# Optimization experiments

Hardware: AMD Instinct MI355X
Metric: run time of the kernel (lower is better)

The kernel has to match this reference:

```python
import jax, jax.numpy as jnp
import numpy as np

N = 30000          # nodes
R = 8              # relations
NUM_BASES = 30     # basis decomposition (fixed in module)
IN_DIM = 256
Z_DIM = 128
HID = Z_DIM * 2
E = N * 16         # edges (avg degree 16)


def setup_inputs() -> dict:
    key = jax.random.key(0)
    ks = jax.random.split(key, 12)
    x = jax.random.normal(ks[0], (N, IN_DIM), jnp.float32)
    edge_index = jax.random.randint(ks[1], (2, E), 0, N, dtype=jnp.int64)
    edge_type = jax.random.randint(ks[2], (E,), 0, R, dtype=jnp.int64)
    s1 = 1.0 / np.sqrt(IN_DIM)
    s2 = 1.0 / np.sqrt(HID)
    sb = 1.0 / np.sqrt(NUM_BASES)
    bases1 = jax.random.normal(ks[3], (NUM_BASES, IN_DIM, HID), jnp.float32) * s1
    comp1 = jax.random.normal(ks[4], (R, NUM_BASES), jnp.float32) * sb
    root1 = jax.random.normal(ks[5], (IN_DIM, HID), jnp.float32) * s1
    bias1 = jnp.zeros((HID,), jnp.float32)
    bases2 = jax.random.normal(ks[6], (NUM_BASES, HID, Z_DIM), jnp.float32) * s2
    comp2 = jax.random.normal(ks[7], (R, NUM_BASES), jnp.float32) * sb
    root2 = jax.random.normal(ks[8], (HID, Z_DIM), jnp.float32) * s2
    bias2 = jnp.zeros((Z_DIM,), jnp.float32)
    return dict(x=x, edge_index=edge_index, edge_type=edge_type,
                bases1=bases1, comp1=comp1, root1=root1, bias1=bias1,
                bases2=bases2, comp2=comp2, root2=root2, bias2=bias2)


def _rgcn_layer(x, src, dst, etype, bases, comp, root, bias):
    # weight[r] = sum_b comp[r,b] * bases[b]  (basis decomposition)
    n = x.shape[0]
    W = jnp.einsum('rb,bio->rio', comp, bases)          # [R, in, out]
    xall = jnp.einsum('ni,rio->nro', x, W)              # [N, R, out] dense transform
    msg = xall[src, etype]                              # [E, out] gather per edge
    seg = dst * R + etype                               # segment = (dst, relation)
    sums = jax.ops.segment_sum(msg, seg, num_segments=n * R)
    cnt = jax.ops.segment_sum(jnp.ones((msg.shape[0],), msg.dtype), seg,
                              num_segments=n * R)
    mean = sums / jnp.maximum(cnt, 1.0)[:, None]        # PyG RGCNConv aggr='mean'
    agg = mean.reshape(n, R, -1).sum(axis=1)            # sum over relations
    return agg + x @ root + bias


def reference(x, edge_index, edge_type, bases1, comp1, root1, bias1,
              bases2, comp2, root2, bias2):
    src, dst = edge_index[0], edge_index[1]
    z = _rgcn_layer(x, src, dst, edge_type, bases1, comp1, root1, bias1)
    z = jax.nn.leaky_relu(z, negative_slope=0.01)
    z = _rgcn_layer(z, src, dst, edge_type, bases2, comp2, root2, bias2)
    return z
```

## Files before the change

kernel.cpp:

```cpp
#include <hip/hip_runtime.h>
#include <hip/hip_bf16.h>
#include <stdint.h>

#define NN     30000
#define MPAD   30080
#define RR     8
#define NBASES 30
#define KD     256
#define EE     480000
#define NSEG   (NN * RR)
#define BK     64
#define CAP    32
#define NC1    2304
#define NC2    1152

typedef unsigned short u16;
typedef __attribute__((ext_vector_type(8))) short bf16x8;
typedef __attribute__((ext_vector_type(4))) float f32x4;

__device__ __forceinline__ u16 f2b(float f) {
  union { float f; uint32_t u; } v; v.f = f;
  return (u16)((v.u + 0x7fffu + ((v.u >> 16) & 1u)) >> 16);
}
__device__ __forceinline__ float b2f(u16 h) {
  union { uint32_t u; float f; } v; v.u = ((uint32_t)h) << 16;
  return v.f;
}

__device__ __forceinline__ void gl_lds16(const void* g, void* l) {
  __builtin_amdgcn_global_load_lds((__attribute__((address_space(1))) void*)g,
                                   (__attribute__((address_space(3))) void*)l,
                                   16, 0, 0);
}

template<int N>
__device__ __forceinline__ void waitcnt_vm() {
  asm volatile("s_waitcnt vmcnt(%0)" :: "n"(N) : "memory");
}

template<int NCOLS>
__global__ __launch_bounds__(512, 2)
void k_gemm_y(const u16* __restrict__ A, const u16* __restrict__ Bn,
              u16* __restrict__ Y) {
  constexpr int NT = 128, MT = 128;
  constexpr int MI = 2, NI = 4;
  constexpr int NKI = KD / BK;
  __shared__ __align__(16) char smem[65536];
  u16 (*Alds)[MT * BK] = (u16(*)[MT * BK])smem;
  u16 (*Blds)[NT * BK] = (u16(*)[NT * BK])(smem + 2 * MT * BK * 2);
  float* eps = (float*)smem;
  const int tid = threadIdx.x;
  const int w = tid >> 6, lane = tid & 63;
  const int bn = blockIdx.x * NT, bm = blockIdx.y * MT;
  const int wm = (w >> 1) * 32;
  const int wn = (w & 1) * 64;
  const int l15 = lane & 15, l4 = lane >> 4;

  f32x4 acc[MI][NI];
  #pragma unroll
  for (int mi = 0; mi < MI; ++mi)
    #pragma unroll
    for (int ni = 0; ni < NI; ++ni) acc[mi][ni] = (f32x4){0.f, 0.f, 0.f, 0.f};

  auto stage = [&](int buf, int k0) {
    #pragma unroll
    for (int it = 0; it < 2; ++it) {
      int chb = it * 512 + w * 64;
      int ch = chb + lane;
      int row = ch >> 3, pc = ch & 7;
      int lc = pc ^ (row & 7);
      gl_lds16(&A[(size_t)(bm + row) * KD + k0 + lc * 8], &Alds[buf][chb * 8]);
    }
    #pragma unroll
    for (int it = 0; it < 2; ++it) {
      int chb = it * 512 + w * 64;
      int ch = chb + lane;
      int row = ch >> 3, pc = ch & 7;
      int lc = pc ^ (row & 7);
      gl_lds16(&Bn[(size_t)(bn + row) * KD + k0 + lc * 8], &Blds[buf][chb * 8]);
    }
  };

  stage(0, 0);
  int buf = 0;
  for (int t = 0; t < NKI; ++t) {
    if (t + 1 < NKI) {
      stage(buf ^ 1, (t + 1) * BK);
      waitcnt_vm<4>();
    } else {
      waitcnt_vm<0>();
    }
    __builtin_amdgcn_s_barrier();
    __builtin_amdgcn_sched_barrier(0);
    #pragma unroll
    for (int s = 0; s < 2; ++s) {
      bf16x8 av[MI], bv[NI];
      #pragma unroll
      for (int mi = 0; mi < MI; ++mi) {
        int row = wm + mi * 16 + l15;
        int pc = (4 * s + l4) ^ (row & 7);
        av[mi] = *(const bf16x8*)&Alds[buf][row * BK + pc * 8];
      }
      #pragma unroll
      for (int ni = 0; ni < NI; ++ni) {
        int row = wn + ni * 16 + l15;
        int pc = (4 * s + l4) ^ (row & 7);
        bv[ni] = *(const bf16x8*)&Blds[buf][row * BK + pc * 8];
      }
      #pragma unroll
      for (int mi = 0; mi < MI; ++mi)
        #pragma unroll
        for (int ni = 0; ni < NI; ++ni)
          acc[mi][ni] = __builtin_amdgcn_mfma_f32_16x16x32_bf16(av[mi], bv[ni], acc[mi][ni], 0, 0, 0);
    }
    asm volatile("s_waitcnt lgkmcnt(0)" ::: "memory");
    __builtin_amdgcn_s_barrier();
    buf ^= 1;
  }

  #pragma unroll
  for (int p = 0; p < 2; ++p) {
    if ((wm >> 6) == p) {
      #pragma unroll
      for (int mi = 0; mi < MI; ++mi)
        #pragma unroll
        for (int ni = 0; ni < NI; ++ni) {
          int col = wn + ni * 16 + l15;
          #pragma unroll
          for (int v = 0; v < 4; ++v) {
            int row = (wm & 63) + mi * 16 + l4 * 4 + v;
            eps[row * 132 + col] = acc[mi][ni][v];
          }
        }
    }
    __syncthreads();
    {
      int row = tid >> 3, oc = tid & 7;
      const float* src = &eps[row * 132 + oc * 16];
      uint4 o[2];
      #pragma unroll
      for (int hh = 0; hh < 2; ++hh) {
        float f0 = src[hh*8+0], f1 = src[hh*8+1], f2 = src[hh*8+2], f3 = src[hh*8+3];
        float f4 = src[hh*8+4], f5 = src[hh*8+5], f6 = src[hh*8+6], f7 = src[hh*8+7];
        o[hh].x = ((uint32_t)f2b(f1) << 16) | (uint32_t)f2b(f0);
        o[hh].y = ((uint32_t)f2b(f3) << 16) | (uint32_t)f2b(f2);
        o[hh].z = ((uint32_t)f2b(f5) << 16) | (uint32_t)f2b(f4);
        o[hh].w = ((uint32_t)f2b(f7) << 16) | (uint32_t)f2b(f6);
      }
      u16* dst = &Y[(size_t)(bm + p * 64 + row) * NCOLS + bn + oc * 16];
      *(uint4*)dst = o[0];
      *(uint4*)(dst + 8) = o[1];
    }
    __syncthreads();
  }
}

template<int D, bool LAST>
__global__ __launch_bounds__(256)
void k_agg(const u16* __restrict__ Y, const int* __restrict__ cnt,
           const int* __restrict__ esrc, const float* __restrict__ bias,
           u16* __restrict__ ob, float* __restrict__ of) {
  constexpr int YW = 9 * D;
  constexpr int CW = D / 32;
  const int tid = threadIdx.x;
  const int h = tid >> 5, ln = tid & 31;
  const int d = blockIdx.x * 8 + h;

  int cn[8];
  {
    int4 c0 = *(const int4*)&cnt[d << 3];
    int4 c1 = *(const int4*)&cnt[(d << 3) + 4];
    cn[0]=c0.x; cn[1]=c0.y; cn[2]=c0.z; cn[3]=c0.w;
    cn[4]=c1.x; cn[5]=c1.y; cn[6]=c1.z; cn[7]=c1.w;
  }
  int4 q[8];
  #pragma unroll
  for (int r = 0; r < 8; ++r)
    q[r] = *(const int4*)&esrc[((d << 3) + r) * CAP];

  float a[CW];
  #pragma unroll
  for (int j = 0; j < CW; ++j) a[j] = 0.f;

  #pragma unroll
  for (int r = 0; r < 8; ++r) {
    int n = cn[r] < CAP ? cn[r] : CAP;
    if (n == 0) continue;
    float t[CW];
    #pragma unroll
    for (int j = 0; j < CW; ++j) t[j] = 0.f;
    const int qsrc[4] = {q[r].x, q[r].y, q[r].z, q[r].w};
    #pragma unroll
    for (int e = 0; e < 4; ++e) {
      if (e < n) {
        int sr = qsrc[e];
        if constexpr (CW == 8) {
          uint4 v = *(const uint4*)&Y[(size_t)sr * YW + r * D + ln * 8];
          t[0]+=b2f((u16)v.x); t[1]+=b2f((u16)(v.x>>16));
          t[2]+=b2f((u16)v.y); t[3]+=b2f((u16)(v.y>>16));
          t[4]+=b2f((u16)v.z); t[5]+=b2f((u16)(v.z>>16));
          t[6]+=b2f((u16)v.w); t[7]+=b2f((u16)(v.w>>16));
        } else {
          uint2 v = *(const uint2*)&Y[(size_t)sr * YW + r * D + ln * 4];
          t[0]+=b2f((u16)v.x); t[1]+=b2f((u16)(v.x>>16));
          t[2]+=b2f((u16)v.y); t[3]+=b2f((u16)(v.y>>16));
        }
      }
    }
    #pragma unroll 1
    for (int e = 4; e < n; ++e) {
      int sr = esrc[((d << 3) + r) * CAP + e];
      if constexpr (CW == 8) {
        uint4 v = *(const uint4*)&Y[(size_t)sr * YW + r * D + ln * 8];
        t[0]+=b2f((u16)v.x); t[1]+=b2f((u16)(v.x>>16));
        t[2]+=b2f((u16)v.y); t[3]+=b2f((u16)(v.y>>16));
        t[4]+=b2f((u16)v.z); t[5]+=b2f((u16)(v.z>>16));
        t[6]+=b2f((u16)v.w); t[7]+=b2f((u16)(v.w>>16));
      } else {
        uint2 v = *(const uint2*)&Y[(size_t)sr * YW + r * D + ln * 4];
        t[0]+=b2f((u16)v.x); t[1]+=b2f((u16)(v.x>>16));
        t[2]+=b2f((u16)v.y); t[3]+=b2f((u16)(v.y>>16));
      }
    }
    float inv = 1.f / (float)n;
    #pragma unroll
    for (int j = 0; j < CW; ++j) a[j] = fmaf(inv, t[j], a[j]);
  }

  if constexpr (CW == 8) {
    uint4 sv = *(const uint4*)&Y[(size_t)d * YW + 8 * D + ln * 8];
    float s[8] = { b2f((u16)sv.x), b2f((u16)(sv.x>>16)),
                   b2f((u16)sv.y), b2f((u16)(sv.y>>16)),
                   b2f((u16)sv.z), b2f((u16)(sv.z>>16)),
                   b2f((u16)sv.w), b2f((u16)(sv.w>>16)) };
    float4 b0 = *(const float4*)&bias[ln * 8];
    float4 b1 = *(const float4*)&bias[ln * 8 + 4];
    float vv[8];
    vv[0]=a[0]+s[0]+b0.x; vv[1]=a[1]+s[1]+b0.y;
    vv[2]=a[2]+s[2]+b0.z; vv[3]=a[3]+s[3]+b0.w;
    vv[4]=a[4]+s[4]+b1.x; vv[5]=a[5]+s[5]+b1.y;
    vv[6]=a[6]+s[6]+b1.z; vv[7]=a[7]+s[7]+b1.w;
    if (!LAST) {
      #pragma unroll
      for (int j = 0; j < 8; ++j) vv[j] = vv[j] > 0.f ? vv[j] : 0.01f * vv[j];
      uint4 o;
      o.x = ((uint32_t)f2b(vv[1]) << 16) | (uint32_t)f2b(vv[0]);
      o.y = ((uint32_t)f2b(vv[3]) << 16) | (uint32_t)f2b(vv[2]);
      o.z = ((uint32_t)f2b(vv[5]) << 16) | (uint32_t)f2b(vv[4]);
      o.w = ((uint32_t)f2b(vv[7]) << 16) | (uint32_t)f2b(vv[6]);
      *(uint4*)&ob[(size_t)d * KD + ln * 8] = o;
    } else {
      float4 o0 = {vv[0], vv[1], vv[2], vv[3]};
      float4 o1 = {vv[4], vv[5], vv[6], vv[7]};
      *(float4*)&of[(size_t)d * 256 + ln * 8] = o0;
      *(float4*)&of[(size_t)d * 256 + ln * 8 + 4] = o1;
    }
  } else {
    uint2 sv = *(const uint2*)&Y[(size_t)d * YW + 8 * D + ln * 4];
    float s[4] = { b2f((u16)sv.x), b2f((u16)(sv.x>>16)),
                   b2f((u16)sv.y), b2f((u16)(sv.y>>16)) };
    float4 b0 = *(const float4*)&bias[ln * 4];
    float vv[4];
    vv[0]=a[0]+s[0]+b0.x; vv[1]=a[1]+s[1]+b0.y;
    vv[2]=a[2]+s[2]+b0.z; vv[3]=a[3]+s[3]+b0.w;
    if (!LAST) {
      #pragma unroll
      for (int j = 0; j < 4; ++j) vv[j] = vv[j] > 0.f ? vv[j] : 0.01f * vv[j];
      uint2 o;
      o.x = ((uint32_t)f2b(vv[1]) << 16) | (uint32_t)f2b(vv[0]);
      o.y = ((uint32_t)f2b(vv[3]) << 16) | (uint32_t)f2b(vv[2]);
      *(uint2*)&ob[(size_t)d * KD + ln * 4] = o;
    } else {
      float4 o = {vv[0], vv[1], vv[2], vv[3]};
      *(float4*)&of[(size_t)d * 128 + ln * 4] = o;
    }
  }
}

__global__ void k_cast_x(const float* __restrict__ x, u16* __restrict__ xb) {
  int t = blockIdx.x * 256 + threadIdx.x;
  if (t < NN * KD / 4) {
    float4 v = ((const float4*)x)[t];
    union { u16 h[4]; uint2 u; } p;
    p.h[0] = f2b(v.x); p.h[1] = f2b(v.y); p.h[2] = f2b(v.z); p.h[3] = f2b(v.w);
    ((uint2*)xb)[t] = p.u;
  }
}

__global__ void k_combineT1(const float* __restrict__ bases, const float* __restrict__ comp,
                            const float* __restrict__ root, u16* __restrict__ Bn) {
  int i = blockIdx.x, rg = blockIdx.y, o = threadIdx.x;
  float v; int j;
  if (rg < RR) {
    float acc = 0.f;
    #pragma unroll
    for (int b = 0; b < NBASES; ++b)
      acc += comp[rg * NBASES + b] * bases[(size_t)b * 65536 + i * 256 + o];
    v = acc; j = rg * 256 + o;
  } else {
    v = root[i * 256 + o]; j = 2048 + o;
  }
  Bn[(size_t)j * KD + i] = f2b(v);
}

__global__ void k_combineT2(const float* __restrict__ bases, const float* __restrict__ comp,
                            const float* __restrict__ root, u16* __restrict__ Bn) {
  int i = blockIdx.x, rg = blockIdx.y, o = threadIdx.x;
  float v; int j;
  if (rg < RR) {
    float acc = 0.f;
    #pragma unroll
    for (int b = 0; b < NBASES; ++b)
      acc += comp[rg * NBASES + b] * bases[(size_t)b * 32768 + i * 128 + o];
    v = acc; j = rg * 128 + o;
  } else {
    v = root[i * 128 + o]; j = 1024 + o;
  }
  Bn[(size_t)j * KD + i] = f2b(v);
}

__global__ void k_bucket_fs(const int* __restrict__ ei, const int* __restrict__ ety,
                            int* __restrict__ cnt, int* __restrict__ esrc) {
  int e = blockIdx.x * 256 + threadIdx.x;
  if (e < EE) {
    int seg = ei[EE + e] * RR + ety[e];
    int pos = atomicAdd(&cnt[seg], 1);
    if (pos < CAP) esrc[seg * CAP + pos] = ei[e];
  }
}

extern "C" void kernel_launch(void* const* d_in, const int* in_sizes, int n_in,
                              void* d_out, int out_size, void* d_ws, size_t ws_size,
                              hipStream_t stream) {
  const float* x      = (const float*)d_in[0];
  const int*   ei     = (const int*)d_in[1];
  const int*   ety    = (const int*)d_in[2];
  const float* bases1 = (const float*)d_in[3];
  const float* comp1  = (const float*)d_in[4];
  const float* root1  = (const float*)d_in[5];
  const float* bias1  = (const float*)d_in[6];
  const float* bases2 = (const float*)d_in[7];
  const float* comp2  = (const float*)d_in[8];
  const float* root2  = (const float*)d_in[9];
  const float* bias2  = (const float*)d_in[10];
  float* out = (float*)d_out;

  char* p = (char*)d_ws;
  auto alloc = [&](size_t bytes) {
    char* q = p; p += (bytes + 255) & ~(size_t)255; return q;
  };
  u16* Y    = (u16*)alloc((size_t)MPAD * NC1 * 2);
  u16* xb   = (u16*)alloc((size_t)MPAD * KD * 2);
  u16* z1b  = (u16*)alloc((size_t)MPAD * KD * 2);
  u16* Bn1  = (u16*)alloc((size_t)NC1 * KD * 2);
  u16* Bn2  = (u16*)alloc((size_t)NC2 * KD * 2);
  int* cnt  = (int*)alloc((size_t)NSEG * 4);
  int* esrc = (int*)alloc((size_t)NSEG * CAP * 4);

  hipMemsetAsync(cnt, 0, (size_t)NSEG * 4, stream);
  k_bucket_fs<<<(EE + 255) / 256, 256, 0, stream>>>(ei, ety, cnt, esrc);

  k_cast_x<<<NN * KD / 4 / 256, 256, 0, stream>>>(x, xb);
  k_combineT1<<<dim3(256, 9), 256, 0, stream>>>(bases1, comp1, root1, Bn1);
  k_combineT2<<<dim3(256, 9), 128, 0, stream>>>(bases2, comp2, root2, Bn2);

  k_gemm_y<NC1><<<dim3(NC1 / 128, MPAD / 128), 512, 0, stream>>>(xb, Bn1, Y);
  k_agg<256, false><<<NN / 8, 256, 0, stream>>>(Y, cnt, esrc, bias1, z1b, nullptr);

  k_gemm_y<NC2><<<dim3(NC2 / 128, MPAD / 128), 512, 0, stream>>>(z1b, Bn2, Y);
  k_agg<128, true><<<NN / 8, 256, 0, stream>>>(Y, cnt, esrc, bias2, nullptr, out);
}
```

Measured before the change: 327.7 us.

## Triple-buffer GEMM K-loop with smaller K tile and new LDS swizzle

The GEMM kernel's K tile shrinks from 64 to 32 and its LDS ring grows from two to three buffers, so loads are issued two iterations ahead. This cuts shared memory per block from 64KB to 48KB and raises the launch-bounds occupancy hint from 2 to 6. The aim is to hide global-load latency and fit more blocks per CU. The cost is twice as many barrier-synchronised iterations, and the 6-block hint may force register spilling with 512-thread blocks.

```diff
diff --git a/kernel.cpp b/kernel.cpp
--- a/kernel.cpp
+++ b/kernel.cpp
@@ -9,7 +9,6 @@
 #define KD     256
 #define EE     480000
 #define NSEG   (NN * RR)
-#define BK     64
 #define CAP    32
 #define NC1    2304
 #define NC2    1152
@@ -39,15 +38,16 @@
 }
 
 template<int NCOLS>
-__global__ __launch_bounds__(512, 2)
+__global__ __launch_bounds__(512, 6)
 void k_gemm_y(const u16* __restrict__ A, const u16* __restrict__ Bn,
               u16* __restrict__ Y) {
   constexpr int NT = 128, MT = 128;
   constexpr int MI = 2, NI = 4;
-  constexpr int NKI = KD / BK;
-  __shared__ __align__(16) char smem[65536];
-  u16 (*Alds)[MT * BK] = (u16(*)[MT * BK])smem;
-  u16 (*Blds)[NT * BK] = (u16(*)[NT * BK])(smem + 2 * MT * BK * 2);
+  constexpr int BKL = 32;
+  constexpr int NKI = KD / BKL;
+  __shared__ __align__(16) char smem[49152];
+  u16 (*Alds)[MT * BKL] = (u16(*)[MT * BKL])smem;
+  u16 (*Blds)[NT * BKL] = (u16(*)[NT * BKL])(smem + 3 * MT * BKL * 2);
   float* eps = (float*)smem;
   const int tid = threadIdx.x;
   const int w = tid >> 6, lane = tid & 63;
@@ -55,6 +55,9 @@
   const int wm = (w >> 1) * 32;
   const int wn = (w & 1) * 64;
   const int l15 = lane & 15, l4 = lane >> 4;
+  const int grow = tid >> 2;
+  const int gpc = tid & 3;
+  const int glc = (gpc - (grow >> 1)) & 3;
 
   f32x4 acc[MI][NI];
   #pragma unroll
@@ -63,49 +66,37 @@
     for (int ni = 0; ni < NI; ++ni) acc[mi][ni] = (f32x4){0.f, 0.f, 0.f, 0.f};
 
   auto stage = [&](int buf, int k0) {
-    #pragma unroll
-    for (int it = 0; it < 2; ++it) {
-      int chb = it * 512 + w * 64;
-      int ch = chb + lane;
-      int row = ch >> 3, pc = ch & 7;
-      int lc = pc ^ (row & 7);
-      gl_lds16(&A[(size_t)(bm + row) * KD + k0 + lc * 8], &Alds[buf][chb * 8]);
-    }
-    #pragma unroll
-    for (int it = 0; it < 2; ++it) {
-      int chb = it * 512 + w * 64;
-      int ch = chb + lane;
-      int row = ch >> 3, pc = ch & 7;
-      int lc = pc ^ (row & 7);
-      gl_lds16(&Bn[(size_t)(bn + row) * KD + k0 + lc * 8], &Blds[buf][chb * 8]);
-    }
+    gl_lds16(&A[(size_t)(bm + grow) * KD + k0 + glc * 8], &Alds[buf][w * 512]);
+    gl_lds16(&Bn[(size_t)(bn + grow) * KD + k0 + glc * 8], &Blds[buf][w * 512]);
   };
 
   stage(0, 0);
-  int buf = 0;
+  stage(1, BKL);
   for (int t = 0; t < NKI; ++t) {
-    if (t + 1 < NKI) {
-      stage(buf ^ 1, (t + 1) * BK);
+    const int bc = t % 3;
+    if (t + 2 < NKI) {
+      stage((t + 2) % 3, (t + 2) * BKL);
       waitcnt_vm<4>();
+    } else if (t + 1 < NKI) {
+      waitcnt_vm<2>();
     } else {
       waitcnt_vm<0>();
     }
     __builtin_amdgcn_s_barrier();
     __builtin_amdgcn_sched_barrier(0);
-    #pragma unroll
-    for (int s = 0; s < 2; ++s) {
+    {
       bf16x8 av[MI], bv[NI];
       #pragma unroll
       for (int mi = 0; mi < MI; ++mi) {
         int row = wm + mi * 16 + l15;
-        int pc = (4 * s + l4) ^ (row & 7);
-        av[mi] = *(const bf16x8*)&Alds[buf][row * BK + pc * 8];
+        int pc = (l4 + (row >> 1)) & 3;
+        av[mi] = *(const bf16x8*)&Alds[bc][row * BKL + pc * 8];
       }
       #pragma unroll
       for (int ni = 0; ni < NI; ++ni) {
         int row = wn + ni * 16 + l15;
-        int pc = (4 * s + l4) ^ (row & 7);
-        bv[ni] = *(const bf16x8*)&Blds[buf][row * BK + pc * 8];
+        int pc = (l4 + (row >> 1)) & 3;
+        bv[ni] = *(const bf16x8*)&Blds[bc][row * BKL + pc * 8];
       }
       #pragma unroll
       for (int mi = 0; mi < MI; ++mi)
@@ -115,7 +106,6 @@
     }
     asm volatile("s_waitcnt lgkmcnt(0)" ::: "memory");
     __builtin_amdgcn_s_barrier();
-    buf ^= 1;
   }
 
   #pragma unroll
```

Result: no change. 328.5 us (+0.3%).

## Merge prep kernels into one launch and use nontemporal stores for GEMM output

Applied to the files above, without the earlier changes.

The four preprocessing kernels (x cast, two basis-combine transposes and edge bucketing) are folded into a single kernel that dispatches on block index ranges. This removes three launch gaps and lets the independent pieces run at the same time. Separately, the GEMM epilogue now writes Y with nontemporal stores, meant to reduce cache pollution from the large intermediate. The risk is that Y is read back soon by the aggregation kernel, so bypassing cache could hurt reuse.

```diff
diff --git a/kernel.cpp b/kernel.cpp
--- a/kernel.cpp
+++ b/kernel.cpp
@@ -17,6 +17,7 @@
 typedef unsigned short u16;
 typedef __attribute__((ext_vector_type(8))) short bf16x8;
 typedef __attribute__((ext_vector_type(4))) float f32x4;
+typedef __attribute__((ext_vector_type(4))) unsigned int u32x4;
 
 __device__ __forceinline__ u16 f2b(float f) {
   union { float f; uint32_t u; } v; v.f = f;
@@ -137,19 +138,19 @@
     {
       int row = tid >> 3, oc = tid & 7;
       const float* src = &eps[row * 132 + oc * 16];
-      uint4 o[2];
+      u32x4 o[2];
       #pragma unroll
       for (int hh = 0; hh < 2; ++hh) {
         float f0 = src[hh*8+0], f1 = src[hh*8+1], f2 = src[hh*8+2], f3 = src[hh*8+3];
         float f4 = src[hh*8+4], f5 = src[hh*8+5], f6 = src[hh*8+6], f7 = src[hh*8+7];
-        o[hh].x = ((uint32_t)f2b(f1) << 16) | (uint32_t)f2b(f0);
-        o[hh].y = ((uint32_t)f2b(f3) << 16) | (uint32_t)f2b(f2);
-        o[hh].z = ((uint32_t)f2b(f5) << 16) | (uint32_t)f2b(f4);
-        o[hh].w = ((uint32_t)f2b(f7) << 16) | (uint32_t)f2b(f6);
+        o[hh][0] = ((uint32_t)f2b(f1) << 16) | (uint32_t)f2b(f0);
+        o[hh][1] = ((uint32_t)f2b(f3) << 16) | (uint32_t)f2b(f2);
+        o[hh][2] = ((uint32_t)f2b(f5) << 16) | (uint32_t)f2b(f4);
+        o[hh][3] = ((uint32_t)f2b(f7) << 16) | (uint32_t)f2b(f6);
       }
       u16* dst = &Y[(size_t)(bm + p * 64 + row) * NCOLS + bn + oc * 16];
-      *(uint4*)dst = o[0];
-      *(uint4*)(dst + 8) = o[1];
+      __builtin_nontemporal_store(o[0], (u32x4*)dst);
+      __builtin_nontemporal_store(o[1], (u32x4*)(dst + 8));
     }
     __syncthreads();
   }
@@ -277,55 +278,65 @@
   }
 }
 
-__global__ void k_cast_x(const float* __restrict__ x, u16* __restrict__ xb) {
-  int t = blockIdx.x * 256 + threadIdx.x;
-  if (t < NN * KD / 4) {
-    float4 v = ((const float4*)x)[t];
-    union { u16 h[4]; uint2 u; } p;
-    p.h[0] = f2b(v.x); p.h[1] = f2b(v.y); p.h[2] = f2b(v.z); p.h[3] = f2b(v.w);
-    ((uint2*)xb)[t] = p.u;
-  }
-}
-
-__global__ void k_combineT1(const float* __restrict__ bases, const float* __restrict__ comp,
-                            const float* __restrict__ root, u16* __restrict__ Bn) {
-  int i = blockIdx.x, rg = blockIdx.y, o = threadIdx.x;
-  float v; int j;
-  if (rg < RR) {
-    float acc = 0.f;
-    #pragma unroll
-    for (int b = 0; b < NBASES; ++b)
-      acc += comp[rg * NBASES + b] * bases[(size_t)b * 65536 + i * 256 + o];
-    v = acc; j = rg * 256 + o;
+#define PB_CAST   7500
+#define PB_CT1    2304
+#define PB_CT2    1152
+#define PB_BKT    1875
+#define PB_TOT    (PB_CAST + PB_CT1 + PB_CT2 + PB_BKT)
+
+__global__ __launch_bounds__(256)
+void k_prep(const float* __restrict__ x, u16* __restrict__ xb,
+            const float* __restrict__ bases1, const float* __restrict__ comp1,
+            const float* __restrict__ root1, u16* __restrict__ Bn1,
+            const float* __restrict__ bases2, const float* __restrict__ comp2,
+            const float* __restrict__ root2, u16* __restrict__ Bn2,
+            const int* __restrict__ ei, const int* __restrict__ ety,
+            int* __restrict__ cnt, int* __restrict__ esrc) {
+  const int b = blockIdx.x, tid = threadIdx.x;
+  if (b < PB_CAST) {
+    int t = b * 256 + tid;
+    if (t < NN * KD / 4) {
+      float4 v = ((const float4*)x)[t];
+      union { u16 h[4]; uint2 u; } p;
+      p.h[0] = f2b(v.x); p.h[1] = f2b(v.y); p.h[2] = f2b(v.z); p.h[3] = f2b(v.w);
+      ((uint2*)xb)[t] = p.u;
+    }
+  } else if (b < PB_CAST + PB_CT1) {
+    int cb = b - PB_CAST;
+    int i = cb & 255, rg = cb >> 8, o = tid;
+    float v; int j;
+    if (rg < RR) {
+      float acc = 0.f;
+      #pragma unroll
+      for (int bb = 0; bb < NBASES; ++bb)
+        acc += comp1[rg * NBASES + bb] * bases1[(size_t)bb * 65536 + i * 256 + o];
+      v = acc; j = rg * 256 + o;
+    } else {
+      v = root1[i * 256 + o]; j = 2048 + o;
+    }
+    Bn1[(size_t)j * KD + i] = f2b(v);
+  } else if (b < PB_CAST + PB_CT1 + PB_CT2) {
+    int cb = b - PB_CAST - PB_CT1;
+    int rg = cb >> 7, ipair = cb & 127;
+    int i = ipair * 2 + (tid >> 7), o = tid & 127;
+    float v; int j;
+    if (rg < RR) {
+      float acc = 0.f;
+      #pragma unroll
+      for (int bb = 0; bb < NBASES; ++bb)
+        acc += comp2[rg * NBASES + bb] * bases2[(size_t)bb * 32768 + i * 128 + o];
+      v = acc; j = rg * 128 + o;
+    } else {
+      v = root2[i * 128 + o]; j = 1024 + o;
+    }
+    Bn2[(size_t)j * KD + i] = f2b(v);
   } else {
-    v = root[i * 256 + o]; j = 2048 + o;
-  }
-  Bn[(size_t)j * KD + i] = f2b(v);
-}
-
-__global__ void k_combineT2(const float* __restrict__ bases, const float* __restrict__ comp,
-                            const float* __restrict__ root, u16* __restrict__ Bn) {
-  int i = blockIdx.x, rg = blockIdx.y, o = threadIdx.x;
-  float v; int j;
-  if (rg < RR) {
-    float acc = 0.f;
-    #pragma unroll
-    for (int b = 0; b < NBASES; ++b)
-      acc += comp[rg * NBASES + b] * bases[(size_t)b * 32768 + i * 128 + o];
-    v = acc; j = rg * 128 + o;
-  } else {
-    v = root[i * 128 + o]; j = 1024 + o;
-  }
-  Bn[(size_t)j * KD + i] = f2b(v);
-}
-
-__global__ void k_bucket_fs(const int* __restrict__ ei, const int* __restrict__ ety,
-                            int* __restrict__ cnt, int* __restrict__ esrc) {
-  int e = blockIdx.x * 256 + threadIdx.x;
-  if (e < EE) {
-    int seg = ei[EE + e] * RR + ety[e];
-    int pos = atomicAdd(&cnt[seg], 1);
-    if (pos < CAP) esrc[seg * CAP + pos] = ei[e];
+    int e = (b - PB_CAST - PB_CT1 - PB_CT2) * 256 + tid;
+    if (e < EE) {
+      int seg = ei[EE + e] * RR + ety[e];
+      int pos = atomicAdd(&cnt[seg], 1);
+      if (pos < CAP) esrc[seg * CAP + pos] = ei[e];
+    }
   }
 }
 
@@ -358,11 +369,9 @@
   int* esrc = (int*)alloc((size_t)NSEG * CAP * 4);
 
   hipMemsetAsync(cnt, 0, (size_t)NSEG * 4, stream);
-  k_bucket_fs<<<(EE + 255) / 256, 256, 0, stream>>>(ei, ety, cnt, esrc);
-
-  k_cast_x<<<NN * KD / 4 / 256, 256, 0, stream>>>(x, xb);
-  k_combineT1<<<dim3(256, 9), 256, 0, stream>>>(bases1, comp1, root1, Bn1);
-  k_combineT2<<<dim3(256, 9), 128, 0, stream>>>(bases2, comp2, root2, Bn2);
+  k_prep<<<PB_TOT, 256, 0, stream>>>(x, xb, bases1, comp1, root1, Bn1,
+                                     bases2, comp2, root2, Bn2,
+                                     ei, ety, cnt, esrc);
 
   k_gemm_y<NC1><<<dim3(NC1 / 128, MPAD / 128), 512, 0, stream>>>(xb, Bn1, Y);
   k_agg<256, false><<<NN / 8, 256, 0, stream>>>(Y, cnt, esrc, bias1, z1b, nullptr);
```

Result: slower. 337.7 us (+3.1%).
